# Kernel optimization log

Measured on AMD Instinct MI355X. Metric: run time of the kernel, lower is better.

Reference implementation:

```python
import jax, jax.numpy as jnp
import numpy as np

H = 12  # num_attention_heads

def setup_inputs() -> dict:
    key = jax.random.key(0)
    ks = jax.random.split(key, 6)
    B, S, D = 2, 2048, 768
    sc = 0.02
    return {
        "hidden_states": jax.random.normal(ks[0], (B, S, D), jnp.float32),
        "Wqr": jax.random.normal(ks[1], (D, D), jnp.float32) * sc,
        "Wqi": jax.random.normal(ks[2], (D, D), jnp.float32) * sc,
        "Wkr": jax.random.normal(ks[3], (D, D), jnp.float32) * sc,
        "Wki": jax.random.normal(ks[4], (D, D), jnp.float32) * sc,
        "Wv": jax.random.normal(ks[5], (D, D), jnp.float32) * sc,
    }

def _heads(x, B, S):
    # [B,S,D] -> [B,H,S,Dh]
    return x.reshape(B, S, H, -1).transpose(0, 2, 1, 3)

def reference(hidden_states, Wqr, Wqi, Wkr, Wki, Wv):
    B, S, D = hidden_states.shape
    Dh = D // H
    x = hidden_states  # real input; imag part is zero
    # complex projections with zero imag input: q = (x@Wqr.T) + i (x@Wqi.T), same for k
    qr = _heads(x @ Wqr.T, B, S)
    qi = _heads(x @ Wqi.T, B, S)
    kr = _heads(x @ Wkr.T, B, S)
    ki = _heads(x @ Wki.T, B, S)
    v = _heads(x @ Wv.T, B, S)
    scale = 1.0 / jnp.sqrt(jnp.float32(Dh))
    # complex QK^H in real arithmetic: s = q @ conj(k)^T
    sr = (jnp.einsum('bhqd,bhkd->bhqk', qr, kr) +
          jnp.einsum('bhqd,bhkd->bhqk', qi, ki)) * scale
    si = (jnp.einsum('bhqd,bhkd->bhqk', qi, kr) -
          jnp.einsum('bhqd,bhkd->bhqk', qr, ki)) * scale
    scores = jnp.sqrt(sr * sr + si * si)  # 'magnitude' variant
    probs = jax.nn.softmax(scores, axis=-1)
    ctx = jnp.einsum('bhqk,bhkd->bhqd', probs, v)
    return ctx.transpose(0, 2, 1, 3).reshape(B, S, D)
```

## Files before the change

### kernel.cpp

```cpp
#include <hip/hip_runtime.h>
#include <cstdint>

typedef short bf16x8 __attribute__((ext_vector_type(8)));
typedef float f32x4 __attribute__((ext_vector_type(4)));

#define MFMA16(a, b, c) __builtin_amdgcn_mfma_f32_16x16x32_bf16((a), (b), (c), 0, 0, 0)

__device__ __forceinline__ void gl16(const unsigned short* g, unsigned short* l) {
  __builtin_amdgcn_global_load_lds(
      (const __attribute__((address_space(1))) unsigned int*)g,
      (__attribute__((address_space(3))) unsigned int*)l, 16, 0, 0);
}

__device__ __forceinline__ unsigned short f2b(float f) {
  union { float f; unsigned int u; } x; x.f = f;
  unsigned int r = x.u + 0x7fffu + ((x.u >> 16) & 1u);
  return (unsigned short)(r >> 16);
}

__device__ __forceinline__ unsigned int pack2(float lo, float hi) {
  union { float f; unsigned int u; } a, b;
  a.f = lo; b.f = hi;
  return ((a.u + 0x8000u) >> 16) | ((b.u + 0x8000u) & 0xffff0000u);
}

#define NB 2
#define NS 2048
#define ND 768
#define NH 12
#define DHD 64
#define MTOK 4096

#define OFF_XB 0
#define OFF_WB 3145728
#define OFF_QK 6094848
#define OFF_VT 18677760

__global__ void cvt_kernel(const float* __restrict__ src,
                           unsigned short* __restrict__ dst, int n4, float scale) {
  int i = blockIdx.x * blockDim.x + threadIdx.x;
  if (i >= n4) return;
  float4 v = ((const float4*)src)[i];
  ushort4 o;
  o.x = f2b(v.x * scale); o.y = f2b(v.y * scale);
  o.z = f2b(v.z * scale); o.w = f2b(v.w * scale);
  ((ushort4*)dst)[i] = o;
}

__global__ void wcvt_kernel(const float* __restrict__ s0, const float* __restrict__ s1,
                            const float* __restrict__ s2, const float* __restrict__ s3,
                            const float* __restrict__ s4, unsigned short* __restrict__ dst,
                            float qs) {
  const int bz = blockIdx.x / 576;
  const int i = (blockIdx.x % 576) * 256 + threadIdx.x;
  const float* src = bz == 0 ? s0 : bz == 1 ? s1 : bz == 2 ? s2 : bz == 3 ? s3 : s4;
  const float scale = bz < 2 ? qs : 1.0f;
  float4 v = ((const float4*)src)[i];
  ushort4 o;
  o.x = f2b(v.x * scale); o.y = f2b(v.y * scale);
  o.z = f2b(v.z * scale); o.w = f2b(v.w * scale);
  ((ushort4*)(dst + bz * 589824))[i] = o;
}

__global__ __launch_bounds__(256) void proj_kernel(
    const unsigned short* __restrict__ Xb, const unsigned short* __restrict__ Wb,
    unsigned short* __restrict__ QK, unsigned short* __restrict__ Vt) {
  __shared__ __align__(16) unsigned short S[17408];
  unsigned short* Xs = S;
  unsigned short* Ws = S + 8192;

  const int lin = blockIdx.x + 6 * (blockIdx.y + 5 * blockIdx.z);
  const int sb = (lin & 7) * 120 + (lin >> 3);
  const int n0 = (sb % 6) * 128;
  const int rem = sb / 6;
  const int z = rem % 5;
  const int m0 = (rem / 5) * 128;

  const unsigned short* Wz = Wb + z * 589824;
  const int tid = threadIdx.x;
  const int lane = tid & 63;
  const int w = tid >> 6;
  const int wm = (w >> 1) * 64;
  const int wn = (w & 1) * 64;
  const int col = lane & 15, quad = lane >> 4;
  const int c7 = col & 7;

  const int lr = lane >> 3;
  const int lc = (lane & 7) ^ (lr & 7);
  const unsigned short* gX = Xb + (m0 + w * 32 + lr) * ND + lc * 8;
  const unsigned short* gW = Wz + (n0 + w * 32 + lr) * ND + lc * 8;
  unsigned short* lX = Xs + (w * 32) * 64;
  unsigned short* lW = Ws + (w * 32) * 64;

  f32x4 acc[4][4] = {};

  for (int k0 = 0; k0 < ND; k0 += 64) {
    __syncthreads();
#pragma unroll
    for (int i = 0; i < 4; i++) {
      gl16(gX + i * (8 * ND) + k0, lX + i * (8 * 64));
      gl16(gW + i * (8 * ND) + k0, lW + i * (8 * 64));
    }
    __syncthreads();
#pragma unroll
    for (int ks = 0; ks < 2; ks++) {
      bf16x8 af[4], bw[4];
#pragma unroll
      for (int t = 0; t < 4; t++) {
        const int fo = (((ks * 4 + quad) ^ c7) * 8);
        af[t] = *(const bf16x8*)(Xs + (wm + t * 16 + col) * 64 + fo);
        bw[t] = *(const bf16x8*)(Ws + (wn + t * 16 + col) * 64 + fo);
      }
#pragma unroll
      for (int mt = 0; mt < 4; mt++)
#pragma unroll
        for (int nt = 0; nt < 4; nt++)
          acc[mt][nt] = MFMA16(af[mt], bw[nt], acc[mt][nt]);
    }
  }

  __syncthreads();
  unsigned short* T = S;

  if (z < 4) {
#pragma unroll
    for (int mt = 0; mt < 4; mt++) {
      int rl = wm + mt * 16 + quad * 4;
#pragma unroll
      for (int nt = 0; nt < 4; nt++) {
        int cl = wn + nt * 16 + col;
#pragma unroll
        for (int r = 0; r < 4; r++) T[(rl + r) * 136 + cl] = f2b(acc[mt][nt][r]);
      }
    }
    __syncthreads();
    unsigned short* out = QK + z * (MTOK * ND);
    const int rr = tid >> 4;
    const int cc = (tid & 15) * 8;
#pragma unroll
    for (int p = 0; p < 8; p++) {
      int row = p * 16 + rr;
      uint4 v = *(const uint4*)(T + row * 136 + cc);
      *(uint4*)(out + (m0 + row) * ND + n0 + cc) = v;
    }
  } else {
#pragma unroll
    for (int mt = 0; mt < 4; mt++) {
      int rl = wm + mt * 16 + quad * 4;
#pragma unroll
      for (int nt = 0; nt < 4; nt++) {
        int cl = wn + nt * 16 + col;
        ushort4 pk;
        pk.x = f2b(acc[mt][nt][0]);
        pk.y = f2b(acc[mt][nt][1]);
        pk.z = f2b(acc[mt][nt][2]);
        pk.w = f2b(acc[mt][nt][3]);
        *(ushort4*)(T + cl * 136 + rl) = pk;
      }
    }
    __syncthreads();
    const int rr = tid >> 4;
    const int cc = (tid & 15) * 8;
    const int b = m0 >> 11;
    const int s_base = m0 & 2047;
#pragma unroll
    for (int p = 0; p < 8; p++) {
      int dhl = p * 16 + rr;
      int c = n0 + dhl;
      int h = c >> 6, dh = c & 63;
      uint4 v = *(const uint4*)(T + dhl * 136 + cc);
      *(uint4*)(Vt + (((b * NH + h) * DHD + dh) * NS + s_base + cc)) = v;
    }
  }
}

__global__ __launch_bounds__(256) void attn_kernel(
    const unsigned short* __restrict__ QK, const unsigned short* __restrict__ Vt,
    float* __restrict__ outp) {
  __shared__ __align__(16) unsigned short Krs[4096];
  __shared__ __align__(16) unsigned short Kis[4096];
  __shared__ __align__(16) unsigned short Vts[4096];
  __shared__ __align__(16) unsigned short Ps[4096];

  const int lin = blockIdx.x + 32 * (blockIdx.y + 12 * blockIdx.z);
  const int sb = (lin & 7) * 96 + (lin >> 3);
  const int qt = sb & 31;
  const int h = (sb >> 5) % 12;
  const int b = sb / 384;
  const int tid = threadIdx.x, lane = tid & 63, w = tid >> 6;
  const int col = lane & 15, quad = lane >> 4;
  const int c7 = col & 7;
  const int jb = quad ^ c7;
  const int f0 = jb * 8, f1 = (jb ^ 4) * 8;

  const unsigned short* Qr = QK;
  const unsigned short* Qi = QK + MTOK * ND;
  const unsigned short* Krp = QK + 2 * MTOK * ND;
  const unsigned short* Kip = QK + 3 * MTOK * ND;

  const int q_tok = b * NS + qt * 64 + w * 16 + col;
  const int qoff = q_tok * ND + h * DHD;

  bf16x8 qrf[2], qif[2], qrn[2];
#pragma unroll
  for (int kk = 0; kk < 2; kk++) {
    qrf[kk] = *(const bf16x8*)(Qr + qoff + kk * 32 + quad * 8);
    qif[kk] = *(const bf16x8*)(Qi + qoff + kk * 32 + quad * 8);
    qrn[kk] = qrf[kk] ^ (short)0x8000;
  }

  const int lr = lane >> 3;
  const int lc = (lane & 7) ^ (lr & 7);
  const unsigned short* gKr = Krp + (b * NS + w * 8 + lr) * ND + h * DHD + lc * 8;
  const unsigned short* gKi = Kip + (b * NS + w * 8 + lr) * ND + h * DHD + lc * 8;
  const unsigned short* gV = Vt + (b * NH + h) * (DHD * NS) + (w * 8 + lr) * NS + lc * 8;
  unsigned short* lKr = Krs + (w * 8) * 64;
  unsigned short* lKi = Kis + (w * 8) * 64;
  unsigned short* lV = Vts + (w * 8) * 64;

  unsigned short* PsW = Ps + w * 1024;

  f32x4 o[4] = {};
  float lrow = 0.f;

  for (int kt = 0; kt < 32; kt++) {
    __syncthreads();
    gl16(gKr, lKr);
    gl16(gKr + 32 * ND, lKr + 2048);
    gl16(gKi, lKi);
    gl16(gKi + 32 * ND, lKi + 2048);
    gl16(gV, lV);
    gl16(gV + 32 * NS, lV + 2048);
    gKr += 64 * ND;
    gKi += 64 * ND;
    gV += 64;
    __syncthreads();

#pragma unroll
    for (int mt = 0; mt < 4; mt++) {
      f32x4 sr = {}, si = {};
      const int rowb = (mt * 16 + col) * 64;
      bf16x8 kr0 = *(const bf16x8*)(Krs + rowb + f0);
      bf16x8 ki0 = *(const bf16x8*)(Kis + rowb + f0);
      bf16x8 kr1 = *(const bf16x8*)(Krs + rowb + f1);
      bf16x8 ki1 = *(const bf16x8*)(Kis + rowb + f1);
      sr = MFMA16(kr0, qrf[0], sr);
      sr = MFMA16(ki0, qif[0], sr);
      si = MFMA16(kr0, qif[0], si);
      si = MFMA16(ki0, qrn[0], si);
      sr = MFMA16(kr1, qrf[1], sr);
      sr = MFMA16(ki1, qif[1], sr);
      si = MFMA16(kr1, qif[1], si);
      si = MFMA16(ki1, qrn[1], si);

      float e0, e1, e2, e3;
      {
        float m0f = __builtin_amdgcn_sqrtf(sr[0] * sr[0] + si[0] * si[0]);
        float m1f = __builtin_amdgcn_sqrtf(sr[1] * sr[1] + si[1] * si[1]);
        float m2f = __builtin_amdgcn_sqrtf(sr[2] * sr[2] + si[2] * si[2]);
        float m3f = __builtin_amdgcn_sqrtf(sr[3] * sr[3] + si[3] * si[3]);
        e0 = __builtin_amdgcn_exp2f(m0f);
        e1 = __builtin_amdgcn_exp2f(m1f);
        e2 = __builtin_amdgcn_exp2f(m2f);
        e3 = __builtin_amdgcn_exp2f(m3f);
      }
      lrow += (e0 + e1) + (e2 + e3);
      uint2 pk;
      pk.x = pack2(e0, e1);
      pk.y = pack2(e2, e3);
      *(uint2*)(PsW + col * 64 + (((mt * 2 + (quad >> 1)) ^ c7) * 8) + (quad & 1) * 4) = pk;
    }
    asm volatile("s_waitcnt lgkmcnt(0)" ::: "memory");

    bf16x8 pb0 = *(const bf16x8*)(PsW + col * 64 + f0);
    bf16x8 pb1 = *(const bf16x8*)(PsW + col * 64 + f1);
#pragma unroll
    for (int dt = 0; dt < 4; dt++) {
      const int rowv = (dt * 16 + col) * 64;
      bf16x8 va0 = *(const bf16x8*)(Vts + rowv + f0);
      bf16x8 va1 = *(const bf16x8*)(Vts + rowv + f1);
      o[dt] = MFMA16(va0, pb0, o[dt]);
      o[dt] = MFMA16(va1, pb1, o[dt]);
    }
  }

  lrow += __shfl_xor(lrow, 16);
  lrow += __shfl_xor(lrow, 32);
  float inv_l = 1.0f / lrow;
  float* op = outp + (size_t)q_tok * ND + h * DHD;
#pragma unroll
  for (int dt = 0; dt < 4; dt++) {
    float4 v;
    v.x = o[dt][0] * inv_l;
    v.y = o[dt][1] * inv_l;
    v.z = o[dt][2] * inv_l;
    v.w = o[dt][3] * inv_l;
    *(float4*)(op + dt * 16 + quad * 4) = v;
  }
}

extern "C" void kernel_launch(void* const* d_in, const int* in_sizes, int n_in,
                              void* d_out, int out_size, void* d_ws, size_t ws_size,
                              hipStream_t stream) {
  const float* X = (const float*)d_in[0];
  unsigned short* ws = (unsigned short*)d_ws;
  unsigned short* Xb = ws + OFF_XB;
  unsigned short* Wb = ws + OFF_WB;
  unsigned short* QK = ws + OFF_QK;
  unsigned short* Vt = ws + OFF_VT;

  const float QSCALE = 0.125f * 1.44269504088896f;

  cvt_kernel<<<3072, 256, 0, stream>>>(X, Xb, 786432, 1.0f);
  wcvt_kernel<<<2880, 256, 0, stream>>>((const float*)d_in[1], (const float*)d_in[2],
                                        (const float*)d_in[3], (const float*)d_in[4],
                                        (const float*)d_in[5], Wb, QSCALE);

  proj_kernel<<<dim3(6, 5, 32), 256, 0, stream>>>(Xb, Wb, QK, Vt);
  attn_kernel<<<dim3(32, 12, 2), 256, 0, stream>>>(QK, Vt, (float*)d_out);
}
```

Before: 193.3 us.

## Double-buffer LDS tiles in projection and attention kernels to overlap loads

Both the projection GEMM and the attention kernel now use two LDS buffers. The next K-tile (and V-tile) is prefetched with global_load_lds while the current tile is consumed by MFMAs, leaving one barrier per iteration instead of two. The aim is to hide global-memory latency behind compute. In exchange, LDS use roughly doubles per block: about 64 KB for proj and 56 KB for attn. That can cut the number of resident blocks per CU and reduce latency hiding through occupancy.

```diff
diff --git a/kernel.cpp b/kernel.cpp
--- a/kernel.cpp
+++ b/kernel.cpp
@@ -65,9 +65,7 @@
 __global__ __launch_bounds__(256) void proj_kernel(
     const unsigned short* __restrict__ Xb, const unsigned short* __restrict__ Wb,
     unsigned short* __restrict__ QK, unsigned short* __restrict__ Vt) {
-  __shared__ __align__(16) unsigned short S[17408];
-  unsigned short* Xs = S;
-  unsigned short* Ws = S + 8192;
+  __shared__ __align__(16) unsigned short S[32768];
 
   const int lin = blockIdx.x + 6 * (blockIdx.y + 5 * blockIdx.z);
   const int sb = (lin & 7) * 120 + (lin >> 3);
@@ -89,27 +87,40 @@
   const int lc = (lane & 7) ^ (lr & 7);
   const unsigned short* gX = Xb + (m0 + w * 32 + lr) * ND + lc * 8;
   const unsigned short* gW = Wz + (n0 + w * 32 + lr) * ND + lc * 8;
-  unsigned short* lX = Xs + (w * 32) * 64;
-  unsigned short* lW = Ws + (w * 32) * 64;
+  unsigned short* lX = S + (w * 32) * 64;
+  unsigned short* lW = S + 16384 + (w * 32) * 64;
 
   f32x4 acc[4][4] = {};
 
-  for (int k0 = 0; k0 < ND; k0 += 64) {
-    __syncthreads();
-#pragma unroll
-    for (int i = 0; i < 4; i++) {
-      gl16(gX + i * (8 * ND) + k0, lX + i * (8 * 64));
-      gl16(gW + i * (8 * ND) + k0, lW + i * (8 * 64));
-    }
-    __syncthreads();
+#pragma unroll
+  for (int i = 0; i < 4; i++) {
+    gl16(gX + i * (8 * ND), lX + i * 512);
+    gl16(gW + i * (8 * ND), lW + i * 512);
+  }
+  __syncthreads();
+
+  int cur = 0;
+  for (int kk = 0; kk < 12; kk++) {
+    if (kk < 11) {
+      const int k0n = (kk + 1) * 64;
+      unsigned short* dX = lX + ((cur ^ 1) * 8192);
+      unsigned short* dW = lW + ((cur ^ 1) * 8192);
+#pragma unroll
+      for (int i = 0; i < 4; i++) {
+        gl16(gX + i * (8 * ND) + k0n, dX + i * 512);
+        gl16(gW + i * (8 * ND) + k0n, dW + i * 512);
+      }
+    }
+    const unsigned short* Xc = S + cur * 8192;
+    const unsigned short* Wc = S + 16384 + cur * 8192;
 #pragma unroll
     for (int ks = 0; ks < 2; ks++) {
       bf16x8 af[4], bw[4];
 #pragma unroll
       for (int t = 0; t < 4; t++) {
         const int fo = (((ks * 4 + quad) ^ c7) * 8);
-        af[t] = *(const bf16x8*)(Xs + (wm + t * 16 + col) * 64 + fo);
-        bw[t] = *(const bf16x8*)(Ws + (wn + t * 16 + col) * 64 + fo);
+        af[t] = *(const bf16x8*)(Xc + (wm + t * 16 + col) * 64 + fo);
+        bw[t] = *(const bf16x8*)(Wc + (wn + t * 16 + col) * 64 + fo);
       }
 #pragma unroll
       for (int mt = 0; mt < 4; mt++)
@@ -117,9 +128,10 @@
         for (int nt = 0; nt < 4; nt++)
           acc[mt][nt] = MFMA16(af[mt], bw[nt], acc[mt][nt]);
     }
-  }
-
-  __syncthreads();
+    __syncthreads();
+    cur ^= 1;
+  }
+
   unsigned short* T = S;
 
   if (z < 4) {
@@ -177,9 +189,9 @@
 __global__ __launch_bounds__(256) void attn_kernel(
     const unsigned short* __restrict__ QK, const unsigned short* __restrict__ Vt,
     float* __restrict__ outp) {
-  __shared__ __align__(16) unsigned short Krs[4096];
-  __shared__ __align__(16) unsigned short Kis[4096];
-  __shared__ __align__(16) unsigned short Vts[4096];
+  __shared__ __align__(16) unsigned short Krs[8192];
+  __shared__ __align__(16) unsigned short Kis[8192];
+  __shared__ __align__(16) unsigned short Vts[8192];
   __shared__ __align__(16) unsigned short Ps[4096];
 
   const int lin = blockIdx.x + 32 * (blockIdx.y + 12 * blockIdx.z);
@@ -214,36 +226,50 @@
   const unsigned short* gKr = Krp + (b * NS + w * 8 + lr) * ND + h * DHD + lc * 8;
   const unsigned short* gKi = Kip + (b * NS + w * 8 + lr) * ND + h * DHD + lc * 8;
   const unsigned short* gV = Vt + (b * NH + h) * (DHD * NS) + (w * 8 + lr) * NS + lc * 8;
-  unsigned short* lKr = Krs + (w * 8) * 64;
-  unsigned short* lKi = Kis + (w * 8) * 64;
-  unsigned short* lV = Vts + (w * 8) * 64;
+  const int st = (w * 8) * 64;
 
   unsigned short* PsW = Ps + w * 1024;
 
   f32x4 o[4] = {};
   float lrow = 0.f;
 
+  gl16(gKr, Krs + st);
+  gl16(gKr + 32 * ND, Krs + st + 2048);
+  gl16(gKi, Kis + st);
+  gl16(gKi + 32 * ND, Kis + st + 2048);
+  gl16(gV, Vts + st);
+  gl16(gV + 32 * NS, Vts + st + 2048);
+  gKr += 64 * ND;
+  gKi += 64 * ND;
+  gV += 64;
+  __syncthreads();
+
+  int cur = 0;
   for (int kt = 0; kt < 32; kt++) {
-    __syncthreads();
-    gl16(gKr, lKr);
-    gl16(gKr + 32 * ND, lKr + 2048);
-    gl16(gKi, lKi);
-    gl16(gKi + 32 * ND, lKi + 2048);
-    gl16(gV, lV);
-    gl16(gV + 32 * NS, lV + 2048);
-    gKr += 64 * ND;
-    gKi += 64 * ND;
-    gV += 64;
-    __syncthreads();
+    if (kt < 31) {
+      const int nb = (cur ^ 1) * 4096;
+      gl16(gKr, Krs + nb + st);
+      gl16(gKr + 32 * ND, Krs + nb + st + 2048);
+      gl16(gKi, Kis + nb + st);
+      gl16(gKi + 32 * ND, Kis + nb + st + 2048);
+      gl16(gV, Vts + nb + st);
+      gl16(gV + 32 * NS, Vts + nb + st + 2048);
+      gKr += 64 * ND;
+      gKi += 64 * ND;
+      gV += 64;
+    }
+    const unsigned short* Kc = Krs + cur * 4096;
+    const unsigned short* Ic = Kis + cur * 4096;
+    const unsigned short* Vc = Vts + cur * 4096;
 
 #pragma unroll
     for (int mt = 0; mt < 4; mt++) {
       f32x4 sr = {}, si = {};
       const int rowb = (mt * 16 + col) * 64;
-      bf16x8 kr0 = *(const bf16x8*)(Krs + rowb + f0);
-      bf16x8 ki0 = *(const bf16x8*)(Kis + rowb + f0);
-      bf16x8 kr1 = *(const bf16x8*)(Krs + rowb + f1);
-      bf16x8 ki1 = *(const bf16x8*)(Kis + rowb + f1);
+      bf16x8 kr0 = *(const bf16x8*)(Kc + rowb + f0);
+      bf16x8 ki0 = *(const bf16x8*)(Ic + rowb + f0);
+      bf16x8 kr1 = *(const bf16x8*)(Kc + rowb + f1);
+      bf16x8 ki1 = *(const bf16x8*)(Ic + rowb + f1);
       sr = MFMA16(kr0, qrf[0], sr);
       sr = MFMA16(ki0, qif[0], sr);
       si = MFMA16(kr0, qif[0], si);
@@ -277,11 +303,13 @@
 #pragma unroll
     for (int dt = 0; dt < 4; dt++) {
       const int rowv = (dt * 16 + col) * 64;
-      bf16x8 va0 = *(const bf16x8*)(Vts + rowv + f0);
-      bf16x8 va1 = *(const bf16x8*)(Vts + rowv + f1);
+      bf16x8 va0 = *(const bf16x8*)(Vc + rowv + f0);
+      bf16x8 va1 = *(const bf16x8*)(Vc + rowv + f1);
       o[dt] = MFMA16(va0, pb0, o[dt]);
       o[dt] = MFMA16(va1, pb1, o[dt]);
     }
+    __syncthreads();
+    cur ^= 1;
   }
 
   lrow += __shfl_xor(lrow, 16);
```

New measurement: 220.8 us. 1.14x slower.
